# Kernel optimization log

Measured on AMD Instinct MI355X. Metric: run time of the kernel, lower is better.

## Reference

```python
import jax, jax.numpy as jnp
import numpy as np

B = 32768
MARGIN = 0.1
P = 2.0          # norm_degree
EPS_BN = 1e-3    # BatchNorm1d eps=0.001
EPS_PD = 1e-6    # F.pairwise_distance eps


def setup_inputs() -> dict:
    key = jax.random.key(0)
    ks = jax.random.split(key, 40)
    W = lambda k, o, i: jax.random.normal(k, (o, i), jnp.float32) * 0.01
    inp = {
        'img_p': jax.random.normal(ks[0], (B, 300), jnp.float32),
        'img_n': jax.random.normal(ks[1], (B, 300), jnp.float32),
        'tag':   jax.random.normal(ks[2], (B, 300), jnp.float32),
        'lat':   jax.random.uniform(ks[3], (B, 1), jnp.float32),
        'lon':   jax.random.uniform(ks[4], (B, 1), jnp.float32),
        # fc_i_1 (Linear 300->1024 + BN)
        'Wi1': W(ks[5], 1024, 300), 'bi1': jnp.zeros(1024), 'gi1': jnp.ones(1024), 'bti1': jnp.zeros(1024),
        # fc_i_2, fc_i_3
        'Wi2': W(ks[6], 1024, 1024), 'bi2': jnp.zeros(1024),
        'Wi3': W(ks[7], 300, 1024), 'bi3': jnp.zeros(300),
        # fc_loc (Linear 2->10 + BN)
        'Wloc': W(ks[8], 10, 2), 'bloc': jnp.zeros(10), 'gloc': jnp.ones(10), 'btloc': jnp.zeros(10),
        # fc_mm_1..3 (Linear + BN), fc_mm_4
        'Wm1': W(ks[9], 1024, 310), 'bm1': jnp.zeros(1024), 'gm1': jnp.ones(1024), 'btm1': jnp.zeros(1024),
        'Wm2': W(ks[10], 1024, 1024), 'bm2': jnp.zeros(1024), 'gm2': jnp.ones(1024), 'btm2': jnp.zeros(1024),
        'Wm3': W(ks[11], 1024, 1024), 'bm3': jnp.zeros(1024), 'gm3': jnp.ones(1024), 'btm3': jnp.zeros(1024),
        'Wm4': W(ks[12], 300, 1024), 'bm4': jnp.zeros(300),
    }
    return inp


def _fc_bn_relu(x, W, b, g, beta):
    # Linear -> BatchNorm1d (training mode, biased batch stats) -> ReLU
    y = x @ W.T + b
    m = jnp.mean(y, axis=0)
    v = jnp.mean((y - m) ** 2, axis=0)
    return jax.nn.relu((y - m) * jax.lax.rsqrt(v + EPS_BN) * g + beta)


def _pairwise_distance(x, y):
    # torch F.pairwise_distance with eps=1e-6
    return jnp.sum(jnp.abs(x - y + EPS_PD) ** P, axis=1) ** (1.0 / P)


def reference(img_p, img_n, tag, lat, lon,
              Wi1, bi1, gi1, bti1, Wi2, bi2, Wi3, bi3,
              Wloc, bloc, gloc, btloc,
              Wm1, bm1, gm1, btm1, Wm2, bm2, gm2, btm2,
              Wm3, bm3, gm3, btm3, Wm4, bm4):
    def img_branch(x):
        x = _fc_bn_relu(x, Wi1, bi1, gi1, bti1)
        x = x @ Wi2.T + bi2
        x = x @ Wi3.T + bi3
        return x
    p = img_branch(img_p)   # [B, 300]
    n = img_branch(img_n)   # [B, 300] (separate BN batch stats, as in torch)
    loc = jnp.concatenate([lat, lon], axis=1)           # [B, 2]
    loc = _fc_bn_relu(loc, Wloc, bloc, gloc, btloc)     # [B, 10]
    a = jnp.concatenate([loc, tag], axis=1)             # [B, 310]
    a = _fc_bn_relu(a, Wm1, bm1, gm1, btm1)
    a = _fc_bn_relu(a, Wm2, bm2, gm2, btm2)
    a = _fc_bn_relu(a, Wm3, bm3, gm3, btm3)
    a = a @ Wm4.T + bm4                                 # [B, 300]
    d_tp = _pairwise_distance(a, p)
    d_tn = _pairwise_distance(a, n)
    # vectorized replacement for the per-element python count loop
    correct = jnp.sum(d_tn - d_tp > MARGIN).astype(jnp.int32).reshape(1)
    return (p, n, a, correct)
```

## Files before the change

### kernel.cpp

```cpp
#include <hip/hip_runtime.h>

typedef _Float16 f16;
typedef _Float16 half8 __attribute__((ext_vector_type(8)));
typedef float f32x4 __attribute__((ext_vector_type(4)));

__device__ __forceinline__ void gl_lds16(const void* g, void* l) {
  __builtin_amdgcn_global_load_lds(
      (__attribute__((address_space(1))) void*)(size_t)g,
      (__attribute__((address_space(3))) void*)l, 16, 0, 0);
}

template <int EPI, int BNA>
__global__ __launch_bounds__(512, 2) void gemm256_k(
    const f16* __restrict__ A, int Ksteps, int KP,
    void* __restrict__ outp, int ldOut, int Ncols,
    float2* __restrict__ partial, int r1, int kz, int oz,
    const f16* __restrict__ B0, const float* __restrict__ bias0,
    const f16* __restrict__ sc0, const f16* __restrict__ sh0,
    const f16* __restrict__ B1, const float* __restrict__ bias1,
    const f16* __restrict__ sc1, const f16* __restrict__ sh1) {
  __shared__ char smem[135168];

  const int t = threadIdx.x;
  const int lane = t & 63;
  const int wave = t >> 6;
  const int wm = wave >> 2, wn = wave & 3;
  const int l16 = lane & 15, lg = lane >> 4;

  int bx = blockIdx.x, by = blockIdx.y;
  {
    const int nwg = gridDim.x * gridDim.y;
    const int wg = bx + gridDim.x * by;
    const int cpx = nwg >> 3;
    const int newid = (wg & 7) * cpx + (wg >> 3);
    bx = newid % gridDim.x;
    by = newid / gridDim.x;
  }
  const int m0 = by * 256;
  const int n0 = bx * 256;

  const f16* Bw = (by >= r1) ? B1 : B0;
  const float* bias = (by >= r1) ? bias1 : bias0;
  const f16* scH = (by >= r1) ? sc1 : sc0;
  const f16* shH = (by >= r1) ? sh1 : sh0;
  const f16* Az = A + (size_t)blockIdx.z * kz;
  Bw += (size_t)blockIdx.z * kz;

  f32x4 acc[8][4] = {};

  const int rA = t >> 2;
  const int g16 = ((t & 3) ^ ((t >> 3) & 3)) * 16;
  const size_t rstep = (size_t)128 * KP * 2;
  const char* gA = (const char*)Az + (size_t)(m0 + rA) * KP * 2 + g16;
  const char* gB = (const char*)Bw + (size_t)(n0 + rA) * KP * 2 + g16;

  auto stage = [&](int slot, int kt) {
    const char* pA = gA + (size_t)kt * 64;
    const char* pB = gB + (size_t)kt * 64;
    char* d = smem + slot * 32768 + t * 16;
    gl_lds16(pA, d);
    gl_lds16(pA + rstep, d + 8192);
    gl_lds16(pB, d + 16384);
    gl_lds16(pB + rstep, d + 24576);
  };

  if constexpr (BNA) {
    if (t < 128)
      gl_lds16((const char*)scH + t * 16, smem + 131072 + t * 16);
    else if (t < 256)
      gl_lds16((const char*)shH + (t - 128) * 16, smem + 133120 + (t - 128) * 16);
  }
  stage(0, 0);
  stage(1, 1);
  stage(2, 2);
  asm volatile("s_waitcnt vmcnt(8)" ::: "memory");
  __builtin_amdgcn_s_barrier();
  asm volatile("" ::: "memory");

  const int xsw = (lg ^ ((l16 >> 1) & 3)) << 4;
  const int oA0 = (wm * 128 + l16) * 64 + xsw;
  const int oB0 = (wn * 64 + l16) * 64 + xsw;

  for (int kt = 0; kt < Ksteps; ++kt) {
    const char* bufA = smem + (kt & 3) * 32768;
    const char* bufB = bufA + 16384;
    half8 af[8], bf0, bf1, scv, shv;
#pragma unroll
    for (int m = 0; m < 8; ++m) af[m] = *(const half8*)(bufA + oA0 + m * 1024);
    bf0 = *(const half8*)(bufB + oB0);
    bf1 = *(const half8*)(bufB + oB0 + 1024);
    if constexpr (BNA) {
      scv = *(const half8*)(smem + 131072 + kt * 64 + lg * 16);
      shv = *(const half8*)(smem + 133120 + kt * 64 + lg * 16);
    }
    if (kt + 3 < Ksteps) {
      const char* pA = gA + (size_t)(kt + 3) * 64;
      char* d = smem + ((kt + 3) & 3) * 32768 + t * 16;
      gl_lds16(pA, d);
      gl_lds16(pA + rstep, d + 8192);
    }
    asm volatile("" ::: "memory");
    __builtin_amdgcn_s_barrier();
    asm volatile("s_waitcnt lgkmcnt(0)" ::: "memory");
    if constexpr (BNA) {
      const half8 zeroh = {};
#pragma unroll
      for (int m = 0; m < 8; ++m)
        af[m] = __builtin_elementwise_max((half8)(af[m] * scv + shv), zeroh);
    }
    __builtin_amdgcn_s_setprio(1);
#pragma unroll
    for (int m = 0; m < 8; ++m) {
      acc[m][0] = __builtin_amdgcn_mfma_f32_16x16x32_f16(af[m], bf0, acc[m][0], 0, 0, 0);
      acc[m][1] = __builtin_amdgcn_mfma_f32_16x16x32_f16(af[m], bf1, acc[m][1], 0, 0, 0);
    }
    __builtin_amdgcn_s_setprio(0);
    half8 bf2 = *(const half8*)(bufB + oB0 + 2048);
    half8 bf3 = *(const half8*)(bufB + oB0 + 3072);
    if (kt + 3 < Ksteps) {
      const char* pB = gB + (size_t)(kt + 3) * 64;
      char* d = smem + ((kt + 3) & 3) * 32768 + t * 16;
      gl_lds16(pB, d + 16384);
      gl_lds16(pB + rstep, d + 24576);
      asm volatile("s_waitcnt vmcnt(8)" ::: "memory");
    } else if (kt == Ksteps - 3) {
      asm volatile("s_waitcnt vmcnt(4)" ::: "memory");
    } else if (kt == Ksteps - 2) {
      asm volatile("s_waitcnt vmcnt(0)" ::: "memory");
    }
    asm volatile("" ::: "memory");
    __builtin_amdgcn_s_barrier();
    asm volatile("s_waitcnt lgkmcnt(0)" ::: "memory");
    __builtin_amdgcn_s_setprio(1);
#pragma unroll
    for (int m = 0; m < 8; ++m) {
      acc[m][2] = __builtin_amdgcn_mfma_f32_16x16x32_f16(af[m], bf2, acc[m][2], 0, 0, 0);
      acc[m][3] = __builtin_amdgcn_mfma_f32_16x16x32_f16(af[m], bf3, acc[m][3], 0, 0, 0);
    }
    __builtin_amdgcn_s_setprio(0);
  }

  __syncthreads();

  float* const swv = (float*)smem + wave * 1152;
  float biasv[4];
#pragma unroll
  for (int n = 0; n < 4; ++n) {
    const int c = n0 + wn * 64 + n * 16 + l16;
    biasv[n] = (bias != nullptr && c < Ncols) ? bias[c] : 0.f;
  }
  float cs[4] = {}, cq[4] = {};
  const int rowr = lane >> 2;
  const int colc = (lane & 3) << 4;

#pragma unroll
  for (int m = 0; m < 8; ++m) {
#pragma unroll
    for (int n = 0; n < 4; ++n)
#pragma unroll
      for (int r = 0; r < 4; ++r) {
        const float v = acc[m][n][r] + biasv[n];
        swv[(lg * 4 + r) * 68 + n * 16 + l16] = v;
        if constexpr (EPI == 0) {
          cs[n] += v;
          cq[n] += v * v;
        }
      }
    asm volatile("s_waitcnt lgkmcnt(0)" ::: "memory");
    const float* sp = swv + rowr * 68 + colc;
    const int grow = m0 + wm * 128 + m * 16 + rowr;
    if constexpr (EPI == 2) {
      float* rp = (float*)outp + (size_t)blockIdx.z * oz + (size_t)grow * ldOut;
#pragma unroll
      for (int j = 0; j < 4; ++j) {
        const int c = n0 + wn * 64 + colc + j * 4;
        const f32x4 v = *(const f32x4*)(sp + j * 4);
        if (c + 3 < Ncols) {
          *(f32x4*)(rp + c) = v;
        } else {
#pragma unroll
          for (int e = 0; e < 4; ++e)
            if (c + e < Ncols) rp[c + e] = v[e];
        }
      }
    } else {
      f16* dp = (f16*)outp + (size_t)grow * ldOut + n0 + wn * 64 + colc;
      const f32x4 v0 = *(const f32x4*)(sp);
      const f32x4 v1 = *(const f32x4*)(sp + 4);
      const f32x4 v2 = *(const f32x4*)(sp + 8);
      const f32x4 v3 = *(const f32x4*)(sp + 12);
      half8 h0, h1;
#pragma unroll
      for (int e = 0; e < 4; ++e) {
        h0[e] = (f16)v0[e];
        h0[4 + e] = (f16)v1[e];
        h1[e] = (f16)v2[e];
        h1[4 + e] = (f16)v3[e];
      }
      *(half8*)dp = h0;
      *(half8*)(dp + 8) = h1;
    }
    asm volatile("s_waitcnt lgkmcnt(0)" ::: "memory");
  }

  if constexpr (EPI == 0) {
    float2* pp = partial + ((size_t)(by * 2 + wm) * 4 + lg) * 1024 + n0 + wn * 64 + l16;
#pragma unroll
    for (int n = 0; n < 4; ++n) pp[n * 16] = make_float2(cs[n], cq[n]);
  }
}

__global__ void bn_red_k(const float2* __restrict__ partial, float2* __restrict__ part2) {
  const int c = blockIdx.x * 256 + threadIdx.x;
  const int chunk = blockIdx.y;
  const float2* p = partial + (size_t)chunk * 64 * 1024 + c;
  float s = 0.f, q = 0.f;
#pragma unroll 4
  for (int i = 0; i < 64; ++i) {
    float2 v = p[(size_t)i * 1024];
    s += v.x;
    q += v.y;
  }
  part2[(size_t)chunk * 1024 + c] = make_float2(s, q);
}

__global__ void bn_fin_k(const float2* __restrict__ part2, int chunkStart, int nchunks,
                         const float* __restrict__ g, const float* __restrict__ beta,
                         f16* __restrict__ scH, f16* __restrict__ shH, float invB) {
  const int c = blockIdx.x * 256 + threadIdx.x;
  float s = 0.f, q = 0.f;
  const float2* p = part2 + (size_t)chunkStart * 1024 + c;
  for (int i = 0; i < nchunks; ++i) {
    float2 v = p[(size_t)i * 1024];
    s += v.x;
    q += v.y;
  }
  float m = s * invB;
  float var = q * invB - m * m;
  float sc = rsqrtf(var + 1e-3f) * g[c];
  scH[c] = (f16)sc;
  shH[c] = (f16)(beta[c] - m * sc);
}

__global__ void bn_fin3_k(const float2* __restrict__ part2, int cps, float invB,
                          const float* __restrict__ g0, const float* __restrict__ b0,
                          f16* __restrict__ so0, f16* __restrict__ sh0,
                          const float* __restrict__ g1, const float* __restrict__ b1,
                          f16* __restrict__ so1, f16* __restrict__ sh1,
                          const float* __restrict__ g2, const float* __restrict__ b2,
                          f16* __restrict__ so2, f16* __restrict__ sh2) {
  const int j = blockIdx.y;
  const float* g = j == 0 ? g0 : (j == 1 ? g1 : g2);
  const float* bt = j == 0 ? b0 : (j == 1 ? b1 : b2);
  f16* so = j == 0 ? so0 : (j == 1 ? so1 : so2);
  f16* sh = j == 0 ? sh0 : (j == 1 ? sh1 : sh2);
  const int c = blockIdx.x * 256 + threadIdx.x;
  float s = 0.f, q = 0.f;
  const float2* p = part2 + (size_t)j * cps * 1024 + c;
  for (int i = 0; i < cps; ++i) {
    float2 v = p[(size_t)i * 1024];
    s += v.x;
    q += v.y;
  }
  float m = s * invB;
  float var = q * invB - m * m;
  float sc = rsqrtf(var + 1e-3f) * g[c];
  so[c] = (f16)sc;
  sh[c] = (f16)(bt[c] - m * sc);
}

__global__ void cvt_all_k(const float* __restrict__ Wi1, const float* __restrict__ Wm1,
                          const float* __restrict__ Wi3, const float* __restrict__ Wm2,
                          const float* __restrict__ Wm3, const float* __restrict__ Wm4,
                          f16* __restrict__ Wi1p, f16* __restrict__ Wm1p,
                          f16* __restrict__ Wi3p, f16* __restrict__ Wm2p,
                          f16* __restrict__ Wm3p, f16* __restrict__ Wm4p) {
  const int k = blockIdx.x * 256 + threadIdx.x;
  const int row = blockIdx.y;
  const float* src;
  f16* dst;
  int n, K, KP, Nreal;
  if (row < 2048) {
    KP = 384;
    if (row < 1024) { src = Wi1; dst = Wi1p; n = row; K = 300; Nreal = 1024; }
    else { src = Wm1; dst = Wm1p; n = row - 1024; K = 310; Nreal = 1024; }
  } else {
    KP = 1024;
    if (row < 2560) { src = Wi3; dst = Wi3p; n = row - 2048; K = 1024; Nreal = 300; }
    else if (row < 3584) { src = Wm2; dst = Wm2p; n = row - 2560; K = 1024; Nreal = 1024; }
    else if (row < 4608) { src = Wm3; dst = Wm3p; n = row - 3584; K = 1024; Nreal = 1024; }
    else { src = Wm4; dst = Wm4p; n = row - 4608; K = 1024; Nreal = 300; }
  }
  if (k >= KP) return;
  float v = (n < Nreal && k < K) ? src[(size_t)n * K + k] : 0.f;
  dst[(size_t)n * KP + k] = (f16)v;
}

__global__ void cvt_wT_k(const float* __restrict__ W, f16* __restrict__ Wt) {
  __shared__ f16 tile[64][65];
  const int bx = blockIdx.x * 64, by = blockIdx.y * 64;
  const int tc = threadIdx.x & 63, tr = threadIdx.x >> 6;
#pragma unroll
  for (int r = tr; r < 64; r += 4)
    tile[r][tc] = (f16)W[(size_t)(by + r) * 1024 + bx + tc];
  __syncthreads();
#pragma unroll
  for (int r = tr; r < 64; r += 4)
    Wt[(size_t)(bx + r) * 1024 + by + tc] = tile[tc][r];
}

__global__ void cvt_in_k(const float* __restrict__ ip, const float* __restrict__ in_,
                         const float* __restrict__ tg, f16* __restrict__ Ain, int B) {
  const int gid = blockIdx.x * 256 + threadIdx.x;
  const int row = gid / 48;
  const int c0 = (gid - row * 48) * 8;
  if (row >= B) return;
  half8 vp = {}, vn = {}, vm = {};
  const float* rp = ip + (size_t)row * 300;
  const float* rn = in_ + (size_t)row * 300;
  const float* rt = tg + (size_t)row * 300;
#pragma unroll
  for (int e = 0; e < 8; ++e) {
    const int c = c0 + e;
    if (c < 300) {
      vp[e] = (f16)rp[c];
      vn[e] = (f16)rn[c];
    }
    if (c >= 10 && c < 310) vm[e] = (f16)rt[c - 10];
  }
  const size_t o = (size_t)row * 384 + c0;
  *(half8*)(Ain + o) = vp;
  *(half8*)(Ain + (size_t)B * 384 + o) = vn;
  *(half8*)(Ain + (size_t)2 * B * 384 + o) = vm;
}

__global__ void fold_red_k(const float* __restrict__ pf, f16* __restrict__ Wf) {
  const int i = blockIdx.x * 256 + threadIdx.x;
  float s = 0.f;
#pragma unroll
  for (int z = 0; z < 8; ++z) s += pf[(size_t)z * 524288 + i];
  Wf[i] = (f16)s;
}

__global__ void bfold_k(const f16* __restrict__ Wi3p, const float* __restrict__ bi2,
                        const float* __restrict__ bi3, float* __restrict__ bf) {
  const int n = blockIdx.x;
  const int t = threadIdx.x;
  float s = 0.f;
  for (int j = t; j < 1024; j += 256) s += (float)Wi3p[(size_t)n * 1024 + j] * bi2[j];
#pragma unroll
  for (int off = 32; off; off >>= 1) s += __shfl_xor(s, off);
  __shared__ float red[4];
  if ((t & 63) == 0) red[t >> 6] = s;
  __syncthreads();
  if (t == 0) bf[n] = red[0] + red[1] + red[2] + red[3] + (n < 300 ? bi3[n] : 0.f);
}

__global__ void loc_stats_k(const float* __restrict__ lat, const float* __restrict__ lon,
                            const float* __restrict__ Wloc, const float* __restrict__ bloc,
                            float* __restrict__ partial) {
  const int t = threadIdx.x;
  const int row = blockIdx.x * 256 + t;
  float la = lat[row], lo = lon[row];
  float s[10], q[10];
#pragma unroll
  for (int j = 0; j < 10; ++j) {
    float y = la * Wloc[j * 2] + lo * Wloc[j * 2 + 1] + bloc[j];
    s[j] = y;
    q[j] = y * y;
  }
#pragma unroll
  for (int j = 0; j < 10; ++j)
    for (int off = 32; off; off >>= 1) {
      s[j] += __shfl_xor(s[j], off);
      q[j] += __shfl_xor(q[j], off);
    }
  __shared__ float red[4][20];
  const int wave = t >> 6, lane = t & 63;
  if (lane == 0) {
#pragma unroll
    for (int j = 0; j < 10; ++j) {
      red[wave][j] = s[j];
      red[wave][10 + j] = q[j];
    }
  }
  __syncthreads();
  if (t < 20) partial[blockIdx.x * 20 + t] = red[0][t] + red[1][t] + red[2][t] + red[3][t];
}

__global__ void loc_fin_k(const float* __restrict__ partial, int nblk,
                          const float* __restrict__ g, const float* __restrict__ beta,
                          float2* __restrict__ ss, float invB) {
  int t = threadIdx.x;
  if (t < 10) {
    float s = 0.f, q = 0.f;
    for (int b = 0; b < nblk; ++b) {
      s += partial[b * 20 + t];
      q += partial[b * 20 + 10 + t];
    }
    float m = s * invB;
    float var = q * invB - m * m;
    float sc = rsqrtf(var + 1e-3f) * g[t];
    ss[t] = make_float2(sc, beta[t] - m * sc);
  }
}

__global__ void loc_write_k(const float* __restrict__ lat, const float* __restrict__ lon,
                            const float* __restrict__ Wloc, const float* __restrict__ bloc,
                            const float2* __restrict__ ss, f16* __restrict__ Am) {
  const int row = blockIdx.x * 256 + threadIdx.x;
  float la = lat[row], lo = lon[row];
  f16* dst = Am + (size_t)row * 384;
#pragma unroll
  for (int j = 0; j < 10; ++j) {
    float y = la * Wloc[j * 2] + lo * Wloc[j * 2 + 1] + bloc[j];
    float2 sv = ss[j];
    dst[j] = (f16)fmaxf(y * sv.x + sv.y, 0.f);
  }
}

__global__ void count_k(const float* __restrict__ P, const float* __restrict__ Nn,
                        const float* __restrict__ Aa, int B, int* __restrict__ cnt) {
  const int gw = (blockIdx.x * blockDim.x + threadIdx.x) >> 6;
  const int lane = threadIdx.x & 63;
  const int nw = (gridDim.x * blockDim.x) >> 6;
  int local = 0;
  for (int row = gw; row < B; row += nw) {
    const float* ar = Aa + (size_t)row * 300;
    const float* pr = P + (size_t)row * 300;
    const float* nr = Nn + (size_t)row * 300;
    float sp = 0.f, sn = 0.f;
    for (int e = lane; e < 300; e += 64) {
      float av = ar[e];
      float d1 = av - pr[e] + 1e-6f;
      float d2 = av - nr[e] + 1e-6f;
      sp += d1 * d1;
      sn += d2 * d2;
    }
#pragma unroll
    for (int off = 32; off; off >>= 1) {
      sp += __shfl_xor(sp, off);
      sn += __shfl_xor(sn, off);
    }
    if (lane == 0 && (sqrtf(sn) - sqrtf(sp) > 0.1f)) ++local;
  }
  if (lane == 0 && local) atomicAdd(cnt, local);
}

__global__ void zero_i32(int* p) {
  if (threadIdx.x == 0 && blockIdx.x == 0) *p = 0;
}
__global__ void write_cnt_k(const int* c, float* o) {
  if (threadIdx.x == 0 && blockIdx.x == 0) *o = (float)(*c);
}

extern "C" void kernel_launch(void* const* d_in, const int* in_sizes, int n_in,
                              void* d_out, int out_size, void* d_ws, size_t ws_size,
                              hipStream_t stream) {
  const float* img_p = (const float*)d_in[0];
  const float* img_n = (const float*)d_in[1];
  const float* tag = (const float*)d_in[2];
  const float* lat = (const float*)d_in[3];
  const float* lon = (const float*)d_in[4];
  const float* Wi1 = (const float*)d_in[5];
  const float* bi1 = (const float*)d_in[6];
  const float* gi1 = (const float*)d_in[7];
  const float* bti1 = (const float*)d_in[8];
  const float* Wi2 = (const float*)d_in[9];
  const float* bi2 = (const float*)d_in[10];
  const float* Wi3 = (const float*)d_in[11];
  const float* bi3 = (const float*)d_in[12];
  const float* Wloc = (const float*)d_in[13];
  const float* bloc = (const float*)d_in[14];
  const float* gloc = (const float*)d_in[15];
  const float* btloc = (const float*)d_in[16];
  const float* Wm1 = (const float*)d_in[17];
  const float* bm1 = (const float*)d_in[18];
  const float* gm1 = (const float*)d_in[19];
  const float* btm1 = (const float*)d_in[20];
  const float* Wm2 = (const float*)d_in[21];
  const float* bm2 = (const float*)d_in[22];
  const float* gm2 = (const float*)d_in[23];
  const float* btm2 = (const float*)d_in[24];
  const float* Wm3 = (const float*)d_in[25];
  const float* bm3 = (const float*)d_in[26];
  const float* gm3 = (const float*)d_in[27];
  const float* btm3 = (const float*)d_in[28];
  const float* Wm4 = (const float*)d_in[29];
  const float* bm4 = (const float*)d_in[30];

  const int B = in_sizes[3];
  const int MT = B / 256;
  float* out = (float*)d_out;
  float* outP = out;
  float* outN = out + (size_t)B * 300;
  float* outA = out + (size_t)2 * B * 300;
  float* outC = out + (size_t)3 * B * 300;

  char* w = (char*)d_ws;
  auto alloc = [&](size_t bytes) {
    char* p = w;
    w += (bytes + 255) & ~(size_t)255;
    return p;
  };

  f16* Wi1p = (f16*)alloc((size_t)1024 * 384 * 2);
  f16* Wm1p = (f16*)alloc((size_t)1024 * 384 * 2);
  f16* Wi2T = (f16*)alloc((size_t)1024 * 1024 * 2);
  f16* Wi3p = (f16*)alloc((size_t)512 * 1024 * 2);
  f16* Wm2p = (f16*)alloc((size_t)1024 * 1024 * 2);
  f16* Wm3p = (f16*)alloc((size_t)1024 * 1024 * 2);
  f16* Wm4p = (f16*)alloc((size_t)512 * 1024 * 2);
  f16* Wfold = (f16*)alloc((size_t)512 * 1024 * 2);
  float* bfold = (float*)alloc(512 * 4);
  f16* ssT = (f16*)alloc(10 * 1024 * 2);
  f16 *scP1 = ssT, *shP1 = ssT + 1024, *scN1 = ssT + 2048, *shN1 = ssT + 3072;
  f16 *scM1 = ssT + 4096, *shM1 = ssT + 5120, *scM2 = ssT + 6144, *shM2 = ssT + 7168;
  f16 *scM3 = ssT + 8192, *shM3 = ssT + 9216;
  float* locpart = (float*)alloc((size_t)(B / 256) * 20 * 4);
  float2* locss = (float2*)alloc(16 * 8);
  int* cnt = (int*)alloc(256);
  f16* Ain = (f16*)alloc((size_t)3 * B * 384 * 2);
  f16* Am = Ain + (size_t)2 * B * 384;
  f16* ACT0 = (f16*)alloc((size_t)3 * B * 1024 * 2);
  f16* ACT0m = ACT0 + (size_t)2 * B * 1024;
  f16* ACT1m = (f16*)alloc((size_t)B * 1024 * 2);
  float2* part = (float2*)alloc((size_t)3072 * 1024 * 8);
  float* partF = (float*)part;
  float2* part2 = (float2*)alloc((size_t)48 * 1024 * 8);
  (void)ws_size;
  (void)out_size;
  (void)n_in;

  const float invB = 1.f / (float)B;
  const int BIG = 1 << 30;

  cvt_all_k<<<dim3(4, 5120), 256, 0, stream>>>(Wi1, Wm1, Wi3, Wm2, Wm3, Wm4,
                                               Wi1p, Wm1p, Wi3p, Wm2p, Wm3p, Wm4p);
  cvt_wT_k<<<dim3(16, 16), 256, 0, stream>>>(Wi2, Wi2T);
  cvt_in_k<<<dim3(B * 48 / 256), 256, 0, stream>>>(img_p, img_n, tag, Ain, B);

  loc_stats_k<<<dim3(B / 256), 256, 0, stream>>>(lat, lon, Wloc, bloc, locpart);
  loc_fin_k<<<dim3(1), 64, 0, stream>>>(locpart, B / 256, gloc, btloc, locss, invB);
  loc_write_k<<<dim3(B / 256), 256, 0, stream>>>(lat, lon, Wloc, bloc, locss, Am);

  bfold_k<<<dim3(512), 256, 0, stream>>>(Wi3p, bi2, bi3, bfold);
  gemm256_k<2, 0><<<dim3(4, 2, 8), 512, 0, stream>>>(
      Wi3p, 4, 1024, partF, 1024, 1024, nullptr, BIG, 128, 524288,
      Wi2T, nullptr, nullptr, nullptr, Wi2T, nullptr, nullptr, nullptr);
  fold_red_k<<<dim3(2048), 256, 0, stream>>>(partF, Wfold);

  gemm256_k<0, 0><<<dim3(4, 3 * MT), 512, 0, stream>>>(
      Ain, 12, 384, ACT0, 1024, 1024, part, 2 * MT, 0, 0,
      Wi1p, bi1, nullptr, nullptr, Wm1p, bm1, nullptr, nullptr);
  bn_red_k<<<dim3(4, 48), 256, 0, stream>>>(part, part2);
  bn_fin3_k<<<dim3(4, 3), 256, 0, stream>>>(
      part2, 16, invB,
      gi1, bti1, scP1, shP1, gi1, bti1, scN1, shN1, gm1, btm1, scM1, shM1);

  gemm256_k<2, 1><<<dim3(2, 2 * MT), 512, 0, stream>>>(
      ACT0, 32, 1024, outP, 300, 300, part, MT, 0, 0,
      Wfold, bfold, scP1, shP1, Wfold, bfold, scN1, shN1);

  gemm256_k<0, 1><<<dim3(4, MT), 512, 0, stream>>>(
      ACT0m, 32, 1024, ACT1m, 1024, 1024, part, BIG, 0, 0,
      Wm2p, bm2, scM1, shM1, Wm2p, bm2, scM1, shM1);
  bn_red_k<<<dim3(4, 16), 256, 0, stream>>>(part, part2);
  bn_fin_k<<<dim3(4), 256, 0, stream>>>(part2, 0, 16, gm2, btm2, scM2, shM2, invB);
  gemm256_k<0, 1><<<dim3(4, MT), 512, 0, stream>>>(
      ACT1m, 32, 1024, ACT0, 1024, 1024, part, BIG, 0, 0,
      Wm3p, bm3, scM2, shM2, Wm3p, bm3, scM2, shM2);
  bn_red_k<<<dim3(4, 16), 256, 0, stream>>>(part, part2);
  bn_fin_k<<<dim3(4), 256, 0, stream>>>(part2, 0, 16, gm3, btm3, scM3, shM3, invB);
  gemm256_k<2, 1><<<dim3(2, MT), 512, 0, stream>>>(
      ACT0, 32, 1024, outA, 300, 300, part, BIG, 0, 0,
      Wm4p, bm4, scM3, shM3, Wm4p, bm4, scM3, shM3);

  zero_i32<<<1, 64, 0, stream>>>(cnt);
  count_k<<<dim3(1024), 256, 0, stream>>>(outP, outN, outA, B, cnt);
  write_cnt_k<<<1, 64, 0, stream>>>(cnt, outC);
}
```

Measured before the change: 712.1 us.

## Store GEMM operands in blocked 256x32 tile layout for contiguous loads

Changes every f16 operand and intermediate activation from row-major to a blocked layout, with 256-row panels split into 32-column chunks stored contiguously. Each k-step stage of the GEMM then loads one contiguous 16KB region instead of 128 strided row fragments. This targets poor DRAM and TLB locality from row-strided global-to-LDS loads. It requires every producer kernel (conversions, fold, loc write, epilogue) to write the new layout, and any missed consumer would read wrong data.

```diff
diff --git a/kernel.cpp b/kernel.cpp
--- a/kernel.cpp
+++ b/kernel.cpp
@@ -43,25 +43,24 @@
   const float* bias = (by >= r1) ? bias1 : bias0;
   const f16* scH = (by >= r1) ? sc1 : sc0;
   const f16* shH = (by >= r1) ? sh1 : sh0;
-  const f16* Az = A + (size_t)blockIdx.z * kz;
-  Bw += (size_t)blockIdx.z * kz;
 
   f32x4 acc[8][4] = {};
 
   const int rA = t >> 2;
   const int g16 = ((t & 3) ^ ((t >> 3) & 3)) * 16;
-  const size_t rstep = (size_t)128 * KP * 2;
-  const char* gA = (const char*)Az + (size_t)(m0 + rA) * KP * 2 + g16;
-  const char* gB = (const char*)Bw + (size_t)(n0 + rA) * KP * 2 + g16;
+  const f16* Ap = A + (size_t)(m0 >> 8) * 256 * KP + (size_t)blockIdx.z * kz;
+  const f16* Bp = Bw + (size_t)(n0 >> 8) * 256 * KP + (size_t)blockIdx.z * kz;
+  const char* gA = (const char*)Ap + rA * 64 + g16;
+  const char* gB = (const char*)Bp + rA * 64 + g16;
 
   auto stage = [&](int slot, int kt) {
-    const char* pA = gA + (size_t)kt * 64;
-    const char* pB = gB + (size_t)kt * 64;
+    const char* pA = gA + (size_t)kt * 16384;
+    const char* pB = gB + (size_t)kt * 16384;
     char* d = smem + slot * 32768 + t * 16;
     gl_lds16(pA, d);
-    gl_lds16(pA + rstep, d + 8192);
+    gl_lds16(pA + 8192, d + 8192);
     gl_lds16(pB, d + 16384);
-    gl_lds16(pB + rstep, d + 24576);
+    gl_lds16(pB + 8192, d + 24576);
   };
 
   if constexpr (BNA) {
@@ -94,10 +93,10 @@
       shv = *(const half8*)(smem + 133120 + kt * 64 + lg * 16);
     }
     if (kt + 3 < Ksteps) {
-      const char* pA = gA + (size_t)(kt + 3) * 64;
+      const char* pA = gA + (size_t)(kt + 3) * 16384;
       char* d = smem + ((kt + 3) & 3) * 32768 + t * 16;
       gl_lds16(pA, d);
-      gl_lds16(pA + rstep, d + 8192);
+      gl_lds16(pA + 8192, d + 8192);
     }
     asm volatile("" ::: "memory");
     __builtin_amdgcn_s_barrier();
@@ -118,10 +117,10 @@
     half8 bf2 = *(const half8*)(bufB + oB0 + 2048);
     half8 bf3 = *(const half8*)(bufB + oB0 + 3072);
     if (kt + 3 < Ksteps) {
-      const char* pB = gB + (size_t)(kt + 3) * 64;
+      const char* pB = gB + (size_t)(kt + 3) * 16384;
       char* d = smem + ((kt + 3) & 3) * 32768 + t * 16;
       gl_lds16(pB, d + 16384);
-      gl_lds16(pB + rstep, d + 24576);
+      gl_lds16(pB + 8192, d + 24576);
       asm volatile("s_waitcnt vmcnt(8)" ::: "memory");
     } else if (kt == Ksteps - 3) {
       asm volatile("s_waitcnt vmcnt(4)" ::: "memory");
@@ -184,7 +183,6 @@
         }
       }
     } else {
-      f16* dp = (f16*)outp + (size_t)grow * ldOut + n0 + wn * 64 + colc;
       const f32x4 v0 = *(const f32x4*)(sp);
       const f32x4 v1 = *(const f32x4*)(sp + 4);
       const f32x4 v2 = *(const f32x4*)(sp + 8);
@@ -197,8 +195,12 @@
         h1[e] = (f16)v2[e];
         h1[4 + e] = (f16)v3[e];
       }
-      *(half8*)dp = h0;
-      *(half8*)(dp + 8) = h1;
+      f16* o16 = (f16*)outp;
+      const size_t dstE = (size_t)(grow >> 8) * 262144 +
+                          (size_t)((n0 >> 5) + wn * 2 + (colc >> 5)) * 8192 +
+                          (size_t)(grow & 255) * 32 + (colc & 31);
+      *(half8*)(o16 + dstE) = h0;
+      *(half8*)(o16 + dstE + 8) = h1;
     }
     asm volatile("s_waitcnt lgkmcnt(0)" ::: "memory");
   }
@@ -293,7 +295,8 @@
   }
   if (k >= KP) return;
   float v = (n < Nreal && k < K) ? src[(size_t)n * K + k] : 0.f;
-  dst[(size_t)n * KP + k] = (f16)v;
+  dst[(size_t)(n >> 8) * 256 * KP + (size_t)(k >> 5) * 8192 +
+      (size_t)(n & 255) * 32 + (k & 31)] = (f16)v;
 }
 
 __global__ void cvt_wT_k(const float* __restrict__ W, f16* __restrict__ Wt) {
@@ -305,8 +308,12 @@
     tile[r][tc] = (f16)W[(size_t)(by + r) * 1024 + bx + tc];
   __syncthreads();
 #pragma unroll
-  for (int r = tr; r < 64; r += 4)
-    Wt[(size_t)(bx + r) * 1024 + by + tc] = tile[tc][r];
+  for (int r = tr; r < 64; r += 4) {
+    const int nr = bx + r;
+    const int kc = by + tc;
+    Wt[(size_t)(nr >> 8) * 262144 + (size_t)(kc >> 5) * 8192 +
+       (size_t)(nr & 255) * 32 + (kc & 31)] = tile[tc][r];
+  }
 }
 
 __global__ void cvt_in_k(const float* __restrict__ ip, const float* __restrict__ in_,
@@ -328,10 +335,12 @@
     }
     if (c >= 10 && c < 310) vm[e] = (f16)rt[c - 10];
   }
-  const size_t o = (size_t)row * 384 + c0;
+  const size_t o = (size_t)(row >> 8) * 98304 + (size_t)(c0 >> 5) * 8192 +
+                   (size_t)(row & 255) * 32 + (c0 & 31);
+  const size_t pstr = (size_t)(B >> 8) * 98304;
   *(half8*)(Ain + o) = vp;
-  *(half8*)(Ain + (size_t)B * 384 + o) = vn;
-  *(half8*)(Ain + (size_t)2 * B * 384 + o) = vm;
+  *(half8*)(Ain + pstr + o) = vn;
+  *(half8*)(Ain + 2 * pstr + o) = vm;
 }
 
 __global__ void fold_red_k(const float* __restrict__ pf, f16* __restrict__ Wf) {
@@ -339,15 +348,19 @@
   float s = 0.f;
 #pragma unroll
   for (int z = 0; z < 8; ++z) s += pf[(size_t)z * 524288 + i];
-  Wf[i] = (f16)s;
+  const int n = i >> 10, k = i & 1023;
+  Wf[(size_t)(n >> 8) * 262144 + (size_t)(k >> 5) * 8192 +
+     (size_t)(n & 255) * 32 + (k & 31)] = (f16)s;
 }
 
 __global__ void bfold_k(const f16* __restrict__ Wi3p, const float* __restrict__ bi2,
                         const float* __restrict__ bi3, float* __restrict__ bf) {
   const int n = blockIdx.x;
   const int t = threadIdx.x;
+  const size_t nb = (size_t)(n >> 8) * 262144 + (size_t)(n & 255) * 32;
   float s = 0.f;
-  for (int j = t; j < 1024; j += 256) s += (float)Wi3p[(size_t)n * 1024 + j] * bi2[j];
+  for (int j = t; j < 1024; j += 256)
+    s += (float)Wi3p[nb + (size_t)(j >> 5) * 8192 + (j & 31)] * bi2[j];
 #pragma unroll
   for (int off = 32; off; off >>= 1) s += __shfl_xor(s, off);
   __shared__ float red[4];
@@ -410,7 +423,7 @@
                             const float2* __restrict__ ss, f16* __restrict__ Am) {
   const int row = blockIdx.x * 256 + threadIdx.x;
   float la = lat[row], lo = lon[row];
-  f16* dst = Am + (size_t)row * 384;
+  f16* dst = Am + (size_t)(row >> 8) * 98304 + (size_t)(row & 255) * 32;
 #pragma unroll
   for (int j = 0; j < 10; ++j) {
     float y = la * Wloc[j * 2] + lo * Wloc[j * 2 + 1] + bloc[j];
@@ -546,7 +559,7 @@
 
   bfold_k<<<dim3(512), 256, 0, stream>>>(Wi3p, bi2, bi3, bfold);
   gemm256_k<2, 0><<<dim3(4, 2, 8), 512, 0, stream>>>(
-      Wi3p, 4, 1024, partF, 1024, 1024, nullptr, BIG, 128, 524288,
+      Wi3p, 4, 1024, partF, 1024, 1024, nullptr, BIG, 32768, 524288,
       Wi2T, nullptr, nullptr, nullptr, Wi2T, nullptr, nullptr, nullptr);
   fold_red_k<<<dim3(2048), 256, 0, stream>>>(partF, Wfold);
 
```

New measurement: 704.2 us. No clear change (-1.1%).
